# Optimization experiments

Hardware: AMD Instinct MI355X
Metric: run time of the kernel (lower is better)

Reference implementation:

```python
import jax, jax.numpy as jnp
import numpy as np

CLIP_LIMIT = 4.0
GRID = (8, 8)
NBINS = 256
B, H, W = 8, 2048, 2048


def setup_inputs() -> dict:
    key = jax.random.key(0)
    img = jax.random.randint(key, (B, H, W), 0, 256).astype(jnp.float32)
    return {"image": img}


def _clahe(image):
    b, h, w = image.shape
    gy, gx = GRID
    th, tw = h // gy, w // gx
    area = th * tw
    # quantize to bins (indices are non-differentiable constants)
    bins = jnp.clip(jax.lax.stop_gradient(image), 0, 255).astype(jnp.int32)  # [B,H,W]

    # ---- per-tile 256-bin histograms via scatter-add ----
    tiles = bins.reshape(b, gy, th, gx, tw).transpose(0, 1, 3, 2, 4)
    tiles = tiles.reshape(b * gy * gx, area)                       # [ntiles, area]
    n = b * gy * gx
    hist = jnp.zeros((n, NBINS), jnp.int32).at[jnp.arange(n)[:, None], tiles].add(1)

    # ---- clip and redistribute excess (OpenCV semantics) ----
    clip_lim = max(int(CLIP_LIMIT * area / NBINS), 1)
    clipped = jnp.minimum(hist, clip_lim)
    excess = (hist - clipped).sum(-1)                              # [ntiles]
    clipped = clipped + (excess // NBINS)[:, None]
    residual = excess % NBINS
    step = jnp.maximum(NBINS // jnp.maximum(residual, 1), 1)       # [ntiles]
    i = jnp.arange(NBINS)
    clipped = clipped + jnp.where(
        (residual[:, None] > 0) & (i[None, :] % step[:, None] == 0), 1, 0)

    # ---- CDF -> per-tile LUT ----
    cdf = jnp.cumsum(clipped, axis=-1)
    lut = jnp.clip(jnp.round(cdf.astype(jnp.float32) * (255.0 / area)), 0.0, 255.0)
    lut = lut.reshape(b, gy, gx, NBINS)                            # [B,gy,gx,256]

    # ---- bilinear interpolation between the 4 neighboring tile LUTs ----
    yf = jnp.arange(h, dtype=jnp.float32) / th - 0.5
    xf = jnp.arange(w, dtype=jnp.float32) / tw - 0.5
    y1f, x1f = jnp.floor(yf), jnp.floor(xf)
    ya, xa = yf - y1f, xf - x1f                                    # frac weights
    y1 = jnp.clip(y1f.astype(jnp.int32), 0, gy - 1)
    y2 = jnp.clip(y1f.astype(jnp.int32) + 1, 0, gy - 1)
    x1 = jnp.clip(x1f.astype(jnp.int32), 0, gx - 1)
    x2 = jnp.clip(x1f.astype(jnp.int32) + 1, 0, gx - 1)

    bi = jnp.arange(b)[:, None, None]        # [B,1,1]
    Y1, Y2 = y1[None, :, None], y2[None, :, None]   # [1,H,1]
    X1, X2 = x1[None, None, :], x2[None, None, :]   # [1,1,W]
    l11 = lut[bi, Y1, X1, bins]
    l12 = lut[bi, Y1, X2, bins]
    l21 = lut[bi, Y2, X1, bins]
    l22 = lut[bi, Y2, X2, bins]

    wy = ya[None, :, None]
    wx = xa[None, None, :]
    res = (l11 * (1 - wx) + l12 * wx) * (1 - wy) + (l21 * (1 - wx) + l22 * wx) * wy
    return jnp.clip(jnp.round(res), 0.0, 255.0)


def reference(image) -> jnp.ndarray:
    return _clahe(image)
```

## Files before the change

kernel.cpp:

```cpp
#include <hip/hip_runtime.h>

#define NB 256
#define CLIP_LIM 1024
#define TSTRIDE 11

template <bool WRITE_BINS>
__global__ __launch_bounds__(1024) void clahe_hist_lut(const float* __restrict__ img,
                                                       float* __restrict__ lut,
                                                       unsigned int* __restrict__ bins) {
    const int t   = blockIdx.x;
    const int b   = t >> 6;
    const int ty  = (t >> 3) & 7;
    const int tx  = t & 7;
    const int tid = threadIdx.x;
    const int wv  = tid >> 6;

    __shared__ int h[16 * NB];
    __shared__ int c[NB];
    __shared__ int s_excess;

    #pragma unroll
    for (int k = 0; k < 4; ++k) h[tid + k * 1024] = 0;
    if (tid == 0) s_excess = 0;
    __syncthreads();

    const float* base = img + ((size_t)b << 22) + (size_t)(ty * 256) * 2048 + tx * 256;
    unsigned int* bbase = bins + ((size_t)b << 20) + ty * 131072 + tx * 64;
    int* hw = &h[wv * NB];

    for (int i = tid; i < 16384; i += 1024) {
        const int r = i >> 6;
        const int q = i & 63;
        const float4 v = *reinterpret_cast<const float4*>(base + (size_t)r * 2048 + q * 4);
        const int b0 = (int)fminf(fmaxf(v.x, 0.f), 255.f);
        const int b1 = (int)fminf(fmaxf(v.y, 0.f), 255.f);
        const int b2 = (int)fminf(fmaxf(v.z, 0.f), 255.f);
        const int b3 = (int)fminf(fmaxf(v.w, 0.f), 255.f);
        atomicAdd(&hw[b0], 1);
        atomicAdd(&hw[b1], 1);
        atomicAdd(&hw[b2], 1);
        atomicAdd(&hw[b3], 1);
        if (WRITE_BINS)
            bbase[r * 512 + q] = (unsigned)b0 | ((unsigned)b1 << 8) |
                                 ((unsigned)b2 << 16) | ((unsigned)b3 << 24);
    }
    __syncthreads();

    int clipped = 0;
    if (tid < NB) {
        int sum = 0;
        #pragma unroll
        for (int w = 0; w < 16; ++w) sum += h[w * NB + tid];
        clipped = min(sum, CLIP_LIM);
        atomicAdd(&s_excess, sum - clipped);
    }
    __syncthreads();

    if (tid < NB) {
        const int excess   = s_excess;
        const int add      = excess >> 8;
        const int residual = excess & 255;
        int step = 256 / (residual > 0 ? residual : 1);
        if (step < 1) step = 1;
        c[tid] = clipped + add + ((residual > 0 && (tid % step) == 0) ? 1 : 0);
    }
    __syncthreads();

    #pragma unroll
    for (int off = 1; off < NB; off <<= 1) {
        int v = 0;
        if (tid < NB && tid >= off) v = c[tid - off];
        __syncthreads();
        if (tid < NB) c[tid] += v;
        __syncthreads();
    }

    if (tid < NB) {
        float lv = rintf((float)c[tid] * (255.0f / 65536.0f));
        lut[t * NB + tid] = fminf(fmaxf(lv, 0.f), 255.f);
    }
}

template <bool USE_BINS>
__global__ __launch_bounds__(256) void clahe_apply(const float* __restrict__ img,
                                                   const unsigned int* __restrict__ bins,
                                                   const float* __restrict__ lut,
                                                   float* __restrict__ out) {
    const int bi  = blockIdx.x;
    const int b   = bi >> 10;
    const int y0  = (bi & 1023) * 2;
    const int tid = threadIdx.x;

    __shared__ float T[2 * NB * TSTRIDE];

    {
        const float yf  = (float)y0 * (1.0f / 256.0f) - 0.5f;
        const float y1f = floorf(yf);
        const int y1 = min(max((int)y1f, 0), 7);
        const int y2 = min(max((int)y1f + 1, 0), 7);
        const float* lb = lut + ((size_t)b << 14);
        float la[8], lc[8];
        #pragma unroll
        for (int xc = 0; xc < 8; ++xc) {
            la[xc] = lb[(y1 * 8 + xc) * NB + tid];
            lc[xc] = lb[(y2 * 8 + xc) * NB + tid];
        }
        #pragma unroll
        for (int r = 0; r < 2; ++r) {
            const float yfr = (float)(y0 + r) * (1.0f / 256.0f) - 0.5f;
            const float ya  = yfr - floorf(yfr);
            float* Tr = &T[r * NB * TSTRIDE + tid * TSTRIDE];
            #pragma unroll
            for (int k = 0; k < 10; ++k) {
                const int kc = (k == 0) ? 0 : ((k - 1 > 7) ? 7 : k - 1);
                Tr[k] = la[kc] * (1.0f - ya) + lc[kc] * ya;
            }
        }
    }
    __syncthreads();

    const size_t imgbase = ((size_t)b << 22) + (size_t)y0 * 2048;
    #pragma unroll
    for (int it = 0; it < 4; ++it) {
        const int r = it >> 1;
        const int i = (it & 1) * 256 + tid;
        const size_t prow = imgbase + (size_t)r * 2048;
        unsigned int w = 0;
        float4 vv;
        if constexpr (USE_BINS) {
            w = bins[(prow >> 2) + i];
        } else {
            vv = *reinterpret_cast<const float4*>(img + prow + i * 4);
        }
        const float* Tr = &T[r * NB * TSTRIDE];
        float res[4];
        #pragma unroll
        for (int j = 0; j < 4; ++j) {
            const int x    = i * 4 + j;
            const float xf = (float)x * (1.0f / 256.0f) - 0.5f;
            const float fl = floorf(xf);
            const float xa = xf - fl;
            const int s    = (int)fl + 1;
            int bn;
            if constexpr (USE_BINS) {
                bn = (w >> (8 * j)) & 255;
            } else {
                const float pv = (j == 0) ? vv.x : (j == 1) ? vv.y : (j == 2) ? vv.z : vv.w;
                bn = (int)fminf(fmaxf(pv, 0.f), 255.f);
            }
            const float* p  = &Tr[bn * TSTRIDE + s];
            const float a   = p[0];
            const float b2  = p[1];
            const float v   = a + (b2 - a) * xa;
            res[j] = fminf(fmaxf(rintf(v), 0.f), 255.f);
        }
        *reinterpret_cast<float4*>(out + prow + i * 4) = make_float4(res[0], res[1], res[2], res[3]);
    }
}

extern "C" void kernel_launch(void* const* d_in, const int* in_sizes, int n_in,
                              void* d_out, int out_size, void* d_ws, size_t ws_size,
                              hipStream_t stream) {
    const float* img = (const float*)d_in[0];
    float* out = (float*)d_out;
    float* lut = (float*)d_ws;
    unsigned int* bins = (unsigned int*)((char*)d_ws + 512 * 1024);
    const size_t need = 512 * 1024 + (size_t)8 * 2048 * 2048;

    if (ws_size >= need) {
        clahe_hist_lut<true><<<512, 1024, 0, stream>>>(img, lut, bins);
        clahe_apply<true><<<8192, 256, 0, stream>>>(img, bins, lut, out);
    } else {
        clahe_hist_lut<false><<<512, 1024, 0, stream>>>(img, lut, nullptr);
        clahe_apply<false><<<8192, 256, 0, stream>>>(img, nullptr, lut, out);
    }
}
```

Baseline: 80.11 us.

## Use 32 padded sub-histograms, nontemporal loads/stores, and 4-row apply blocks

```diff
diff --git a/kernel.cpp b/kernel.cpp
--- a/kernel.cpp
+++ b/kernel.cpp
@@ -3,8 +3,12 @@
 #define NB 256
 #define CLIP_LIM 1024
 #define TSTRIDE 11
+#define HSTRIDE 264
+#define NSUB 32
+#define ROWS 4
 
-template <bool WRITE_BINS>
+typedef float f32x4 __attribute__((ext_vector_type(4)));
+
 __global__ __launch_bounds__(1024) void clahe_hist_lut(const float* __restrict__ img,
                                                        float* __restrict__ lut,
                                                        unsigned int* __restrict__ bins) {
@@ -13,25 +17,29 @@
     const int ty  = (t >> 3) & 7;
     const int tx  = t & 7;
     const int tid = threadIdx.x;
-    const int wv  = tid >> 6;
+    const int sub = ((tid >> 6) << 1) | (tid & 1);
 
-    __shared__ int h[16 * NB];
+    __shared__ int h[NSUB * HSTRIDE];
     __shared__ int c[NB];
     __shared__ int s_excess;
 
     #pragma unroll
-    for (int k = 0; k < 4; ++k) h[tid + k * 1024] = 0;
+    for (int k = 0; k < 9; ++k) {
+        const int idx = tid + k * 1024;
+        if (idx < NSUB * HSTRIDE) h[idx] = 0;
+    }
     if (tid == 0) s_excess = 0;
     __syncthreads();
 
     const float* base = img + ((size_t)b << 22) + (size_t)(ty * 256) * 2048 + tx * 256;
     unsigned int* bbase = bins + ((size_t)b << 20) + ty * 131072 + tx * 64;
-    int* hw = &h[wv * NB];
+    int* hw = &h[sub * HSTRIDE];
 
     for (int i = tid; i < 16384; i += 1024) {
         const int r = i >> 6;
         const int q = i & 63;
-        const float4 v = *reinterpret_cast<const float4*>(base + (size_t)r * 2048 + q * 4);
+        const f32x4 v = __builtin_nontemporal_load(
+            reinterpret_cast<const f32x4*>(base + (size_t)r * 2048 + q * 4));
         const int b0 = (int)fminf(fmaxf(v.x, 0.f), 255.f);
         const int b1 = (int)fminf(fmaxf(v.y, 0.f), 255.f);
         const int b2 = (int)fminf(fmaxf(v.z, 0.f), 255.f);
@@ -40,9 +48,8 @@
         atomicAdd(&hw[b1], 1);
         atomicAdd(&hw[b2], 1);
         atomicAdd(&hw[b3], 1);
-        if (WRITE_BINS)
-            bbase[r * 512 + q] = (unsigned)b0 | ((unsigned)b1 << 8) |
-                                 ((unsigned)b2 << 16) | ((unsigned)b3 << 24);
+        bbase[r * 512 + q] = (unsigned)b0 | ((unsigned)b1 << 8) |
+                             ((unsigned)b2 << 16) | ((unsigned)b3 << 24);
     }
     __syncthreads();
 
@@ -50,7 +57,7 @@
     if (tid < NB) {
         int sum = 0;
         #pragma unroll
-        for (int w = 0; w < 16; ++w) sum += h[w * NB + tid];
+        for (int w = 0; w < NSUB; ++w) sum += h[w * HSTRIDE + tid];
         clipped = min(sum, CLIP_LIM);
         atomicAdd(&s_excess, sum - clipped);
     }
@@ -81,17 +88,15 @@
     }
 }
 
-template <bool USE_BINS>
-__global__ __launch_bounds__(256) void clahe_apply(const float* __restrict__ img,
-                                                   const unsigned int* __restrict__ bins,
+__global__ __launch_bounds__(256) void clahe_apply(const unsigned int* __restrict__ bins,
                                                    const float* __restrict__ lut,
                                                    float* __restrict__ out) {
     const int bi  = blockIdx.x;
-    const int b   = bi >> 10;
-    const int y0  = (bi & 1023) * 2;
+    const int b   = bi >> 9;
+    const int y0  = (bi & 511) * ROWS;
     const int tid = threadIdx.x;
 
-    __shared__ float T[2 * NB * TSTRIDE];
+    __shared__ float T[ROWS * NB * TSTRIDE];
 
     {
         const float yf  = (float)y0 * (1.0f / 256.0f) - 0.5f;
@@ -106,7 +111,7 @@
             lc[xc] = lb[(y2 * 8 + xc) * NB + tid];
         }
         #pragma unroll
-        for (int r = 0; r < 2; ++r) {
+        for (int r = 0; r < ROWS; ++r) {
             const float yfr = (float)(y0 + r) * (1.0f / 256.0f) - 0.5f;
             const float ya  = yfr - floorf(yfr);
             float* Tr = &T[r * NB * TSTRIDE + tid * TSTRIDE];
@@ -121,17 +126,11 @@
 
     const size_t imgbase = ((size_t)b << 22) + (size_t)y0 * 2048;
     #pragma unroll
-    for (int it = 0; it < 4; ++it) {
+    for (int it = 0; it < 2 * ROWS; ++it) {
         const int r = it >> 1;
         const int i = (it & 1) * 256 + tid;
         const size_t prow = imgbase + (size_t)r * 2048;
-        unsigned int w = 0;
-        float4 vv;
-        if constexpr (USE_BINS) {
-            w = bins[(prow >> 2) + i];
-        } else {
-            vv = *reinterpret_cast<const float4*>(img + prow + i * 4);
-        }
+        const unsigned int w = bins[(prow >> 2) + i];
         const float* Tr = &T[r * NB * TSTRIDE];
         float res[4];
         #pragma unroll
@@ -141,20 +140,15 @@
             const float fl = floorf(xf);
             const float xa = xf - fl;
             const int s    = (int)fl + 1;
-            int bn;
-            if constexpr (USE_BINS) {
-                bn = (w >> (8 * j)) & 255;
-            } else {
-                const float pv = (j == 0) ? vv.x : (j == 1) ? vv.y : (j == 2) ? vv.z : vv.w;
-                bn = (int)fminf(fmaxf(pv, 0.f), 255.f);
-            }
-            const float* p  = &Tr[bn * TSTRIDE + s];
-            const float a   = p[0];
-            const float b2  = p[1];
-            const float v   = a + (b2 - a) * xa;
+            const int bn   = (w >> (8 * j)) & 255;
+            const float* p = &Tr[bn * TSTRIDE + s];
+            const float a  = p[0];
+            const float b2 = p[1];
+            const float v  = a + (b2 - a) * xa;
             res[j] = fminf(fmaxf(rintf(v), 0.f), 255.f);
         }
-        *reinterpret_cast<float4*>(out + prow + i * 4) = make_float4(res[0], res[1], res[2], res[3]);
+        const f32x4 o = { res[0], res[1], res[2], res[3] };
+        __builtin_nontemporal_store(o, reinterpret_cast<f32x4*>(out + prow + i * 4));
     }
 }
 
@@ -165,13 +159,7 @@
     float* out = (float*)d_out;
     float* lut = (float*)d_ws;
     unsigned int* bins = (unsigned int*)((char*)d_ws + 512 * 1024);
-    const size_t need = 512 * 1024 + (size_t)8 * 2048 * 2048;
 
-    if (ws_size >= need) {
-        clahe_hist_lut<true><<<512, 1024, 0, stream>>>(img, lut, bins);
-        clahe_apply<true><<<8192, 256, 0, stream>>>(img, bins, lut, out);
-    } else {
-        clahe_hist_lut<false><<<512, 1024, 0, stream>>>(img, lut, nullptr);
-        clahe_apply<false><<<8192, 256, 0, stream>>>(img, nullptr, lut, out);
-    }
+    clahe_hist_lut<<<512, 1024, 0, stream>>>(img, lut, bins);
+    clahe_apply<<<8 * (2048 / ROWS), 256, 0, stream>>>(bins, lut, out);
 }
```

Result: no change. 79.79 us (-0.4%).
